# Kernel optimization log

Measured on AMD Instinct MI355X. Metric: run time of the kernel, lower is better.

## Reference

```python
import jax, jax.numpy as jnp
import numpy as np

N_FFT = 1024
HOP = 256
N_MELS = 128
SR = 16000
EPS = 1e-6
S = 0.025
ALPHA = 0.98
DELTA = 2.0
R = 0.5


def make_mel_fb():
    # Faithful port of F2M._init_buffers (onesided=True)
    n_freq = N_FFT // 2 + 1
    f_max = SR // 2
    m_min = 0.0
    m_max = 2595.0 * np.log10(1.0 + f_max / 700.0)
    m_pts = np.linspace(m_min, m_max, N_MELS + 2)
    f_pts = 700.0 * (10.0 ** (m_pts / 2595.0) - 1.0)
    bins = np.floor((n_freq - 1) * 2 * f_pts / SR).astype(np.int64)
    fb = np.zeros((n_freq, N_MELS), dtype=np.float32)
    for m in range(1, N_MELS + 1):
        a, b, c = int(bins[m - 1]), int(bins[m]), int(bins[m + 1])
        if a != b:
            fb[a:b, m - 1] = (np.arange(a, b) - a) / (b - a)
        if b != c:
            fb[b:c, m - 1] = (c - np.arange(b, c)) / (c - b)
    return jnp.asarray(fb)


def setup_inputs() -> dict:
    key = jax.random.key(0)
    x = jax.random.normal(key, (32, 160000), dtype=jnp.float32)
    return {"x": x, "fb": make_mel_fb()}


def reference(x, fb):
    # torch.stft with center=True (default), rectangular window (window=None)
    pad = N_FFT // 2
    xp = jnp.pad(x, ((0, 0), (pad, pad)), mode="reflect")
    n_frames = (xp.shape[1] - N_FFT) // HOP + 1
    idx = jnp.arange(n_frames)[:, None] * HOP + jnp.arange(N_FFT)[None, :]
    frames = xp[:, idx]                       # [B, T, n_fft]
    spec = jnp.abs(jnp.fft.rfft(frames, axis=-1))   # magnitude, [B, T, F]
    mel = jnp.einsum("btf,fm->btm", spec, fb)       # [B, T, M]

    # PCEN EMA smoother: M_0 = x_0, M_t = (1-s) M_{t-1} + s x_t
    def step(m_prev, frame):
        m = (1.0 - S) * m_prev + S * frame
        return m, m

    x0 = mel[:, 0, :]                               # [B, M]
    _, ms = jax.lax.scan(step, x0, jnp.swapaxes(mel[:, 1:, :], 0, 1))
    M = jnp.concatenate([x0[:, None, :], jnp.swapaxes(ms, 0, 1)], axis=1)

    out = (mel / (M + EPS) ** ALPHA + DELTA) ** R - DELTA ** R
    return out
```

## Files before the change

### kernel.cpp

```cpp
#include <hip/hip_runtime.h>
#include <math.h>

#define NMELS   128
#define NFRAMES 626
#define NPAIRS  313
#define NBATCH  32
#define LSAMP   160000
#define NFREQ   513
#define PPB     4
#define NBLK    ((NPAIRS + PPB - 1) / PPB)
#define NCHUNK  NBLK

struct Bins { int v[NMELS + 2]; };

__device__ __forceinline__ int refl(int i) {
    if (i < 0) i = -i;
    else if (i >= LSAMP) i = 2 * LSAMP - 2 - i;
    return i;
}

__device__ __forceinline__ float2 cadd(float2 a, float2 b){return make_float2(a.x+b.x, a.y+b.y);}
__device__ __forceinline__ float2 csub(float2 a, float2 b){return make_float2(a.x-b.x, a.y-b.y);}
__device__ __forceinline__ float2 cmul(float2 a, float2 b){
    return make_float2(fmaf(a.x,b.x,-a.y*b.y), fmaf(a.x,b.y,a.y*b.x));
}
__device__ __forceinline__ float2 cmulnegi(float2 a){return make_float2(a.y, -a.x);}

__device__ __forceinline__ void dft16(float2* z) {
    const float2 W1 = make_float2( 0.92387953251f, -0.38268343236f);
    const float2 W2 = make_float2( 0.70710678119f, -0.70710678119f);
    const float2 W3 = make_float2( 0.38268343236f, -0.92387953251f);
    const float2 W6 = make_float2(-0.70710678119f, -0.70710678119f);
    const float2 W9 = make_float2(-0.92387953251f,  0.38268343236f);
    float2 g[16];
    #pragma unroll
    for (int q = 0; q < 4; q++) {
        float2 t0=z[q], t1=z[4+q], t2=z[8+q], t3=z[12+q];
        float2 A=cadd(t0,t2), B=csub(t0,t2), C=cadd(t1,t3), D=csub(t1,t3);
        g[q]    = cadd(A,C);
        g[4+q]  = make_float2(B.x + D.y, B.y - D.x);
        g[8+q]  = csub(A,C);
        g[12+q] = make_float2(B.x - D.y, B.y + D.x);
    }
    g[4+1] =cmul(g[4+1], W1); g[4+2] =cmul(g[4+2], W2); g[4+3] =cmul(g[4+3], W3);
    g[8+1] =cmul(g[8+1], W2); g[8+2] =cmulnegi(g[8+2]); g[8+3] =cmul(g[8+3], W6);
    g[12+1]=cmul(g[12+1],W3); g[12+2]=cmul(g[12+2],W6);  g[12+3]=cmul(g[12+3],W9);
    #pragma unroll
    for (int r = 0; r < 4; r++) {
        float2 t0=g[4*r], t1=g[4*r+1], t2=g[4*r+2], t3=g[4*r+3];
        float2 A=cadd(t0,t2), B=csub(t0,t2), C=cadd(t1,t3), D=csub(t1,t3);
        z[r]    = cadd(A,C);
        z[r+4]  = make_float2(B.x + D.y, B.y - D.x);
        z[r+8]  = csub(A,C);
        z[r+12] = make_float2(B.x - D.y, B.y + D.x);
    }
}

__global__ __launch_bounds__(256, 4)
void fft_mel_kernel(const float* __restrict__ x, float* __restrict__ mel,
                    float* __restrict__ S, Bins bins) {
    __shared__ float2 wbuf[PPB][1088];

    const int tid = threadIdx.x;
    const int w   = tid >> 6;
    const int u   = tid & 63;
    const int P   = blockIdx.x;
    const int b   = blockIdx.y;
    const int p   = P * PPB + w;

    float acc[4];

    if (p < NPAIRS) {
        float2* buf  = wbuf[w];
        float*  spec = (float*)&wbuf[w][0];

        const float* xb = x + (size_t)b * LSAMP;
        const int base = 512 * p - 512;
        #pragma unroll
        for (int j = 0; j < 16; j++) {
            const int i = 64 * j + u;
            buf[i] = make_float2(xb[refl(base + i)], xb[refl(base + i + 256)]);
        }

        float2 z[16];

        #pragma unroll
        for (int a = 0; a < 16; a++) z[a] = buf[64*a + u];
        dft16(z);
        {
            float s, c; __sincosf(-(float)M_PI * (float)u * (1.0f/512.0f), &s, &c);
            float2 w1 = make_float2(c, s), wk = w1;
            #pragma unroll
            for (int k = 1; k < 16; k++) { z[k] = cmul(z[k], wk); wk = cmul(wk, w1); }
        }
        #pragma unroll
        for (int k = 0; k < 16; k++) buf[17*u + k] = z[k];

        const int k1 = u >> 2, bp = u & 3;
        #pragma unroll
        for (int a = 0; a < 16; a++) z[a] = buf[68*a + 17*bp + k1];
        dft16(z);
        {
            float s, c; __sincosf(-(float)M_PI * (float)bp * (1.0f/32.0f), &s, &c);
            float2 w1 = make_float2(c, s), wk = w1;
            #pragma unroll
            for (int k = 1; k < 16; k++) { z[k] = cmul(z[k], wk); wk = cmul(wk, w1); }
        }
        #pragma unroll
        for (int k = 0; k < 16; k++) buf[68*k + 17*bp + k1] = z[k];

        #pragma unroll
        for (int j = 0; j < 4; j++) {
            const int c = 64*j + u;
            const int kk1 = c & 15, k2a = c >> 4;
            #pragma unroll
            for (int bq = 0; bq < 4; bq++) z[4*j + bq] = buf[68*k2a + 17*bq + kk1];
        }
        #pragma unroll
        for (int j = 0; j < 4; j++) {
            const int kbase = u + 64*j;
            float2 t0=z[4*j], t1=z[4*j+1], t2=z[4*j+2], t3=z[4*j+3];
            float2 A=cadd(t0,t2), B=csub(t0,t2), C=cadd(t1,t3), D=csub(t1,t3);
            buf[kbase]       = cadd(A,C);
            buf[kbase + 256] = make_float2(B.x + D.y, B.y - D.x);
            buf[kbase + 512] = csub(A,C);
            buf[kbase + 768] = make_float2(B.x - D.y, B.y + D.x);
        }

        float m0[9], m1[9];
        #pragma unroll
        for (int j = 0; j < 9; j++) {
            const int k = 64*j + u;
            if (k <= 512) {
                const int nk = (1024 - k) & 1023;
                float2 Zk = buf[k], Zn = buf[nk];
                float ar = Zk.x + Zn.x, ai = Zk.y - Zn.y;
                float br = Zk.y + Zn.y, bi = Zn.x - Zk.x;
                m0[j] = 0.5f * sqrtf(ar*ar + ai*ai);
                m1[j] = 0.5f * sqrtf(br*br + bi*bi);
            }
        }
        #pragma unroll
        for (int j = 0; j < 9; j++) {
            const int k = 64*j + u;
            if (k <= 512) { spec[k] = m0[j]; spec[NFREQ + k] = m1[j]; }
        }

        const int r = u & 31, pf = u >> 5;
        const float* sp = spec + pf * NFREQ;
        #pragma unroll
        for (int i = 0; i < 4; i++) {
            const int mm = 32*i + r;
            const int a = bins.v[mm], bb = bins.v[mm+1], c = bins.v[mm+2];
            float a0 = 0.f;
            if (bb > a) {
                float s = 0.f;
                for (int f = a; f < bb; f++) s = fmaf(sp[f], (float)(f - a), s);
                a0 += s / (float)(bb - a);
            }
            if (c > bb) {
                float s = 0.f;
                for (int f = bb; f < c; f++) s = fmaf(sp[f], (float)(c - f), s);
                a0 += s / (float)(c - bb);
            }
            acc[i] = a0;
            mel[((size_t)b * NFRAMES + 2*p + pf) * NMELS + mm] = a0;
        }
    }
    __syncthreads();

    float* melst = (float*)&wbuf[0][544];
    if (p < NPAIRS) {
        const int r = u & 31, pf = u >> 5;
        const int fl = 2*w + pf;
        #pragma unroll
        for (int i = 0; i < 4; i++) melst[fl*NMELS + 32*i + r] = acc[i];
    }
    __syncthreads();

    if (tid < NMELS) {
        const int t0 = P * 8;
        const int nf = (NFRAMES - t0 < 8) ? NFRAMES - t0 : 8;
        float s = 0.f;
        for (int f = 0; f < nf; f++) {
            float v = melst[f*NMELS + tid];
            s = (t0 + f == 0) ? v : fmaf(0.975f, s, 0.025f * v);
        }
        S[((size_t)b * NCHUNK + P) * NMELS + tid] = s;
    }
}

__global__ __launch_bounds__(256)
void pcen_scan(const float* __restrict__ S, float* __restrict__ Mstart) {
    const int idx = blockIdx.x * 256 + threadIdx.x;
    const int m = idx & 127;
    const int b = idx >> 7;
    if (b >= NBATCH) return;

    float D8; { float d = 0.975f; d *= d; d *= d; d *= d; D8 = d; }

    const size_t base = (size_t)b * NCHUNK * NMELS + m;
    float M = 0.f;
    #pragma unroll 8
    for (int c = 0; c < NCHUNK; c++) {
        Mstart[base + (size_t)c * NMELS] = M;
        M = fmaf(D8, M, S[base + (size_t)c * NMELS]);
    }
}

__global__ __launch_bounds__(128)
void pcen_out(const float* __restrict__ mel, const float* __restrict__ Mstart,
              float* __restrict__ out) {
    const int m = threadIdx.x;
    const int c = blockIdx.x;
    const int b = blockIdx.y;

    float M = Mstart[((size_t)b * NCHUNK + c) * NMELS + m];

    const int t0 = c * 8;
    const int tend = (t0 + 8 < NFRAMES) ? t0 + 8 : NFRAMES;
    const float* mp = mel + (size_t)b * NFRAMES * NMELS + m;
    float*       op = out + (size_t)b * NFRAMES * NMELS + m;
    #pragma unroll 8
    for (int t = t0; t < tend; t++) {
        float v = mp[(size_t)t * NMELS];
        M = (t == 0) ? v : fmaf(0.975f, M, 0.025f * v);
        float den = __powf(M + 1e-6f, 0.98f);
        op[(size_t)t * NMELS] = sqrtf(v / den + 2.0f) - 1.41421356237f;
    }
}

extern "C" void kernel_launch(void* const* d_in, const int* in_sizes, int n_in,
                              void* d_out, int out_size, void* d_ws, size_t ws_size,
                              hipStream_t stream) {
    const float* x  = (const float*)d_in[0];
    float* out = (float*)d_out;

    float* mel    = (float*)d_ws;
    float* S      = mel + (size_t)NBATCH * NFRAMES * NMELS;
    float* Mstart = S   + (size_t)NBATCH * NCHUNK * NMELS;

    Bins bins;
    {
        const double m_max = 2595.0 * log10(1.0 + 8000.0 / 700.0);
        const double step  = m_max / 129.0;
        for (int i = 0; i < NMELS + 2; i++) {
            double mv = (i == NMELS + 1) ? m_max : (double)i * step;
            double f  = 700.0 * (pow(10.0, mv / 2595.0) - 1.0);
            bins.v[i] = (int)floor((double)(NFREQ - 1) * 2.0 * f / 16000.0);
        }
    }

    dim3 grid1(NBLK, NBATCH);
    fft_mel_kernel<<<grid1, 256, 0, stream>>>(x, mel, S, bins);

    pcen_scan<<<(NBATCH * NMELS + 255) / 256, 256, 0, stream>>>(S, Mstart);

    dim3 grid3(NCHUNK, NBATCH);
    pcen_out<<<grid3, 128, 0, stream>>>(mel, Mstart, out);
}
```

Before: 122.2 us.

## Halve FFT block size, vectorize frame loads, fuse last radix-4 with magnitude

```diff
diff --git a/kernel.cpp b/kernel.cpp
--- a/kernel.cpp
+++ b/kernel.cpp
@@ -7,7 +7,7 @@
 #define NBATCH  32
 #define LSAMP   160000
 #define NFREQ   513
-#define PPB     4
+#define PPB     2
 #define NBLK    ((NPAIRS + PPB - 1) / PPB)
 #define NCHUNK  NBLK
 
@@ -56,7 +56,35 @@
     }
 }
 
-__global__ __launch_bounds__(256, 4)
+__device__ __forceinline__ void twpow(float2 w1, float2* tw) {
+    tw[1] = w1;
+    tw[2] = cmul(tw[1], tw[1]);
+    tw[4] = cmul(tw[2], tw[2]);
+    tw[8] = cmul(tw[4], tw[4]);
+    tw[3] = cmul(tw[2], tw[1]);
+    tw[5] = cmul(tw[4], tw[1]);
+    tw[6] = cmul(tw[4], tw[2]);
+    tw[7] = cmul(tw[4], tw[3]);
+    #pragma unroll
+    for (int k = 9; k < 16; k++) tw[k] = cmul(tw[8], tw[k-8]);
+}
+
+__device__ __forceinline__ void dft4v(const float2* t, float2* Z) {
+    float2 A=cadd(t[0],t[2]), B=csub(t[0],t[2]), C=cadd(t[1],t[3]), D=csub(t[1],t[3]);
+    Z[0] = cadd(A,C);
+    Z[1] = make_float2(B.x + D.y, B.y - D.x);
+    Z[2] = csub(A,C);
+    Z[3] = make_float2(B.x - D.y, B.y + D.x);
+}
+
+__device__ __forceinline__ void emitmag(float* spec, int k, float2 Zk, float2 Zn) {
+    float ar = Zk.x + Zn.x, ai = Zk.y - Zn.y;
+    float br = Zk.y + Zn.y, bi = Zn.x - Zk.x;
+    spec[k]         = 0.5f * sqrtf(ar*ar + ai*ai);
+    spec[NFREQ + k] = 0.5f * sqrtf(br*br + bi*bi);
+}
+
+__global__ __launch_bounds__(128, 4)
 void fft_mel_kernel(const float* __restrict__ x, float* __restrict__ mel,
                     float* __restrict__ S, Bins bins) {
     __shared__ float2 wbuf[PPB][1088];
@@ -76,22 +104,36 @@
 
         const float* xb = x + (size_t)b * LSAMP;
         const int base = 512 * p - 512;
-        #pragma unroll
-        for (int j = 0; j < 16; j++) {
-            const int i = 64 * j + u;
-            buf[i] = make_float2(xb[refl(base + i)], xb[refl(base + i + 256)]);
-        }
-
-        float2 z[16];
+        if (base >= 0 && base + 1280 <= LSAMP) {
+            const float4* xv4 = (const float4*)(xb + base);
+            #pragma unroll
+            for (int j = 0; j < 4; j++) {
+                float4 v0 = xv4[64*j + u];
+                float4 v1 = xv4[64*j + u + 64];
+                const int i = 4 * (64*j + u);
+                buf[i]   = make_float2(v0.x, v1.x);
+                buf[i+1] = make_float2(v0.y, v1.y);
+                buf[i+2] = make_float2(v0.z, v1.z);
+                buf[i+3] = make_float2(v0.w, v1.w);
+            }
+        } else {
+            #pragma unroll
+            for (int j = 0; j < 16; j++) {
+                const int i = 64 * j + u;
+                buf[i] = make_float2(xb[refl(base + i)], xb[refl(base + i + 256)]);
+            }
+        }
+
+        float2 z[16], tw[16];
 
         #pragma unroll
         for (int a = 0; a < 16; a++) z[a] = buf[64*a + u];
         dft16(z);
         {
             float s, c; __sincosf(-(float)M_PI * (float)u * (1.0f/512.0f), &s, &c);
-            float2 w1 = make_float2(c, s), wk = w1;
-            #pragma unroll
-            for (int k = 1; k < 16; k++) { z[k] = cmul(z[k], wk); wk = cmul(wk, w1); }
+            twpow(make_float2(c, s), tw);
+            #pragma unroll
+            for (int k = 1; k < 16; k++) z[k] = cmul(z[k], tw[k]);
         }
         #pragma unroll
         for (int k = 0; k < 16; k++) buf[17*u + k] = z[k];
@@ -102,48 +144,42 @@
         dft16(z);
         {
             float s, c; __sincosf(-(float)M_PI * (float)bp * (1.0f/32.0f), &s, &c);
-            float2 w1 = make_float2(c, s), wk = w1;
-            #pragma unroll
-            for (int k = 1; k < 16; k++) { z[k] = cmul(z[k], wk); wk = cmul(wk, w1); }
+            twpow(make_float2(c, s), tw);
+            #pragma unroll
+            for (int k = 1; k < 16; k++) z[k] = cmul(z[k], tw[k]);
         }
         #pragma unroll
         for (int k = 0; k < 16; k++) buf[68*k + 17*bp + k1] = z[k];
 
-        #pragma unroll
-        for (int j = 0; j < 4; j++) {
-            const int c = 64*j + u;
-            const int kk1 = c & 15, k2a = c >> 4;
-            #pragma unroll
-            for (int bq = 0; bq < 4; bq++) z[4*j + bq] = buf[68*k2a + 17*bq + kk1];
-        }
-        #pragma unroll
-        for (int j = 0; j < 4; j++) {
-            const int kbase = u + 64*j;
-            float2 t0=z[4*j], t1=z[4*j+1], t2=z[4*j+2], t3=z[4*j+3];
-            float2 A=cadd(t0,t2), B=csub(t0,t2), C=cadd(t1,t3), D=csub(t1,t3);
-            buf[kbase]       = cadd(A,C);
-            buf[kbase + 256] = make_float2(B.x + D.y, B.y - D.x);
-            buf[kbase + 512] = csub(A,C);
-            buf[kbase + 768] = make_float2(B.x - D.y, B.y + D.x);
-        }
-
-        float m0[9], m1[9];
-        #pragma unroll
-        for (int j = 0; j < 9; j++) {
-            const int k = 64*j + u;
-            if (k <= 512) {
-                const int nk = (1024 - k) & 1023;
-                float2 Zk = buf[k], Zn = buf[nk];
-                float ar = Zk.x + Zn.x, ai = Zk.y - Zn.y;
-                float br = Zk.y + Zn.y, bi = Zn.x - Zk.x;
-                m0[j] = 0.5f * sqrtf(ar*ar + ai*ai);
-                m1[j] = 0.5f * sqrtf(br*br + bi*bi);
-            }
-        }
-        #pragma unroll
-        for (int j = 0; j < 9; j++) {
-            const int k = 64*j + u;
-            if (k <= 512) { spec[k] = m0[j]; spec[NFREQ + k] = m1[j]; }
+        const int cA0 = u;
+        const int cB0 = (u == 0) ? 128 : 256 - u;
+        const int cA1 = 64 + u;
+        const int cB1 = 192 - u;
+        float2 tA0[4], tB0[4], tA1[4], tB1[4];
+        #pragma unroll
+        for (int bq = 0; bq < 4; bq++) {
+            tA0[bq] = buf[68*(cA0 >> 4) + 17*bq + (cA0 & 15)];
+            tB0[bq] = buf[68*(cB0 >> 4) + 17*bq + (cB0 & 15)];
+            tA1[bq] = buf[68*(cA1 >> 4) + 17*bq + (cA1 & 15)];
+            tB1[bq] = buf[68*(cB1 >> 4) + 17*bq + (cB1 & 15)];
+        }
+        {
+            float2 ZA[4], ZB[4];
+            dft4v(tA0, ZA); dft4v(tB0, ZB);
+            #pragma unroll
+            for (int j = 0; j < 2; j++) {
+                float2 znA = (u == 0) ? ZA[(4-j) & 3] : ZB[3-j];
+                emitmag(spec, cA0 + 256*j, ZA[j], znA);
+                float2 znB = (u == 0) ? ZB[3-j] : ZA[3-j];
+                emitmag(spec, cB0 + 256*j, ZB[j], znB);
+            }
+            if (u == 0) emitmag(spec, 512, ZA[2], ZA[2]);
+            dft4v(tA1, ZA); dft4v(tB1, ZB);
+            #pragma unroll
+            for (int j = 0; j < 2; j++) {
+                emitmag(spec, cA1 + 256*j, ZA[j], ZB[3-j]);
+                emitmag(spec, cB1 + 256*j, ZB[j], ZA[3-j]);
+            }
         }
 
         const int r = u & 31, pf = u >> 5;
@@ -169,7 +205,7 @@
     }
     __syncthreads();
 
-    float* melst = (float*)&wbuf[0][544];
+    float* melst = (float*)&wbuf[1][0];
     if (p < NPAIRS) {
         const int r = u & 31, pf = u >> 5;
         const int fl = 2*w + pf;
@@ -178,9 +214,9 @@
     }
     __syncthreads();
 
-    if (tid < NMELS) {
-        const int t0 = P * 8;
-        const int nf = (NFRAMES - t0 < 8) ? NFRAMES - t0 : 8;
+    {
+        const int t0 = P * 4;
+        const int nf = (NFRAMES - t0 < 4) ? NFRAMES - t0 : 4;
         float s = 0.f;
         for (int f = 0; f < nf; f++) {
             float v = melst[f*NMELS + tid];
@@ -197,14 +233,14 @@
     const int b = idx >> 7;
     if (b >= NBATCH) return;
 
-    float D8; { float d = 0.975f; d *= d; d *= d; d *= d; D8 = d; }
+    float D4; { float d = 0.975f; d *= d; d *= d; D4 = d; }
 
     const size_t base = (size_t)b * NCHUNK * NMELS + m;
     float M = 0.f;
     #pragma unroll 8
     for (int c = 0; c < NCHUNK; c++) {
         Mstart[base + (size_t)c * NMELS] = M;
-        M = fmaf(D8, M, S[base + (size_t)c * NMELS]);
+        M = fmaf(D4, M, S[base + (size_t)c * NMELS]);
     }
 }
 
@@ -217,11 +253,11 @@
 
     float M = Mstart[((size_t)b * NCHUNK + c) * NMELS + m];
 
-    const int t0 = c * 8;
-    const int tend = (t0 + 8 < NFRAMES) ? t0 + 8 : NFRAMES;
+    const int t0 = c * 4;
+    const int tend = (t0 + 4 < NFRAMES) ? t0 + 4 : NFRAMES;
     const float* mp = mel + (size_t)b * NFRAMES * NMELS + m;
     float*       op = out + (size_t)b * NFRAMES * NMELS + m;
-    #pragma unroll 8
+    #pragma unroll 4
     for (int t = t0; t < tend; t++) {
         float v = mp[(size_t)t * NMELS];
         M = (t == 0) ? v : fmaf(0.975f, M, 0.025f * v);
@@ -252,7 +288,7 @@
     }
 
     dim3 grid1(NBLK, NBATCH);
-    fft_mel_kernel<<<grid1, 256, 0, stream>>>(x, mel, S, bins);
+    fft_mel_kernel<<<grid1, 128, 0, stream>>>(x, mel, S, bins);
 
     pcen_scan<<<(NBATCH * NMELS + 255) / 256, 256, 0, stream>>>(S, Mstart);
 
```

Result: slower. 128.7 us (+5.4%).
